# Performance work log

Measured on AMD Instinct MI355X. Metric: run time of the kernel, lower is better.

Reference implementation:

```python
import jax, jax.numpy as jnp
import numpy as np

TEMPERATURE = 0.05


def _hungarian_max(C):
    """Jonker-Volgenant shortest-augmenting-path LAP on a square numpy matrix.
    Returns col index matched to each row, maximizing total cost
    (equivalent to scipy.optimize.linear_sum_assignment(C, maximize=True))."""
    cost = -np.asarray(C, dtype=np.float64)  # minimize negated cost
    n = cost.shape[0]
    INF = np.inf
    u = np.zeros(n + 1)
    v = np.zeros(n + 1)
    p = np.zeros(n + 1, dtype=np.int64)   # p[j] = row matched to column j (1-based)
    way = np.zeros(n + 1, dtype=np.int64)
    for i in range(1, n + 1):
        p[0] = i
        j0 = 0
        minv = np.full(n + 1, INF)
        used = np.zeros(n + 1, dtype=bool)
        while True:
            used[j0] = True
            i0 = p[j0]
            delta = INF
            j1 = -1
            for j in range(1, n + 1):
                if not used[j]:
                    cur = cost[i0 - 1, j - 1] - u[i0] - v[j]
                    if cur < minv[j]:
                        minv[j] = cur
                        way[j] = j0
                    if minv[j] < delta:
                        delta = minv[j]
                        j1 = j
            for j in range(n + 1):
                if used[j]:
                    u[p[j]] += delta
                    v[j] -= delta
                else:
                    minv[j] -= delta
            j0 = j1
            if p[j0] == 0:
                break
        while j0:
            j1 = way[j0]
            p[j0] = p[j1]
            j0 = j1
    col_of_row = np.zeros(n, dtype=np.int64)
    for j in range(1, n + 1):
        col_of_row[p[j] - 1] = j - 1
    return col_of_row


def setup_inputs() -> dict:
    key = jax.random.key(0)
    k1, k2, k3 = jax.random.split(key, 3)
    B, K, D = 256, 16, 1024
    return {
        "outputs": jax.random.normal(k1, (B, K, D), dtype=jnp.float32),
        "positive_embeddings": jax.random.normal(k2, (B, K, D), dtype=jnp.float32),
        "negative_embeddings": jax.random.normal(k3, (B, K, D), dtype=jnp.float32),
    }


def reference(outputs, positive_embeddings, negative_embeddings):
    B, K, D = outputs.shape
    o = outputs.reshape(B * K, D) / TEMPERATURE          # (BK, D)
    emb = jnp.concatenate(
        [positive_embeddings.reshape(B * K, D),
         negative_embeddings.reshape(B * K, D)], axis=0)  # (2BK, D)
    sim = jnp.einsum("bd,cd->bc", o, emb)                 # (BK, 2BK)
    sim = jax.nn.log_softmax(sim, axis=1)
    # i-th KxK diagonal block: rows [K*i, K*(i+1)), cols [K*i, K*(i+1))
    idx = jnp.arange(B)
    blocks = sim.reshape(B, K, 2 * B, K)[idx, :, idx, :]  # (B, K, K)
    # Hungarian matching (detached in original -> no grad through assignment)
    blk_np = np.asarray(jax.device_get(jax.lax.stop_gradient(blocks)))
    cols = jnp.asarray(np.stack([_hungarian_max(blk_np[b]) for b in range(B)]))  # (B, K)
    matched = blocks[idx[:, None], jnp.arange(K)[None, :], cols]  # (B, K)
    # per-sample mean of -matched, then mean over batch == overall mean
    return jnp.mean(-matched)
```

## Files before the change

### kernel.cpp

```cpp
#include <hip/hip_runtime.h>
#include <hip/hip_bf16.h>
#include <math.h>

#define Ddim 1024
#define Mrows 4096
#define Ncols 8192
#define BM 128
#define BN 128
#define BK 32
#define NCS 64
#define CS 64
#define RT (Mrows / BM)
#define KITERS (Ddim / BK)
#define NSOLVE 256
#define SCALE 20.0f
#define ARR_ELEMS (Mrows * Ddim)
#define DOTS_PAD 132

typedef __bf16 bf16_t;
typedef __bf16 bf16x8 __attribute__((ext_vector_type(8)));
typedef float f32x4 __attribute__((ext_vector_type(4)));

#define LOAD16_TO_LDS(g, l)                                                  \
  __builtin_amdgcn_global_load_lds(                                          \
      (const __attribute__((address_space(1))) void*)(g),                    \
      (__attribute__((address_space(3))) void*)(l), 16, 0, 0)

__device__ __forceinline__ int rdlane_i(int v, int lane) {
  return __builtin_amdgcn_readlane(v, lane);
}
__device__ __forceinline__ float rdlane_f(float v, int lane) {
  return __int_as_float(__builtin_amdgcn_readlane(__float_as_int(v), lane));
}
__device__ __forceinline__ float rdfirst_f(float v) {
  return __int_as_float(__builtin_amdgcn_readfirstlane(__float_as_int(v)));
}

template <int N>
__device__ __forceinline__ void argmin_ror(float& cand, int& idx) {
  const float ov = __int_as_float(__builtin_amdgcn_update_dpp(
      __float_as_int(cand), __float_as_int(cand), 0x120 | N, 0xf, 0xf, false));
  const int oi = __builtin_amdgcn_update_dpp(idx, idx, 0x120 | N, 0xf, 0xf, false);
  if (ov < cand || (ov == cand && oi < idx)) { cand = ov; idx = oi; }
}

__global__ __launch_bounds__(256) void cvt_kernel(
    const float* __restrict__ o, const float* __restrict__ pos,
    const float* __restrict__ neg, bf16_t* __restrict__ ob,
    bf16_t* __restrict__ pb, bf16_t* __restrict__ nb,
    float* __restrict__ out)
{
  if (blockIdx.x == 0 && threadIdx.x == 0) out[0] = 0.f;
  const int idx = blockIdx.x * 256 + threadIdx.x;
  const int seg = idx >> 19;
  const int off = idx & ((1 << 19) - 1);
  const float* src = (seg == 0) ? o : (seg == 1) ? pos : neg;
  bf16_t* dst = (seg == 0) ? ob : (seg == 1) ? pb : nb;
  const float4 v0 = *(const float4*)(src + (size_t)off * 8);
  const float4 v1 = *(const float4*)(src + (size_t)off * 8 + 4);
  bf16x8 r = {(bf16_t)v0.x, (bf16_t)v0.y, (bf16_t)v0.z, (bf16_t)v0.w,
              (bf16_t)v1.x, (bf16_t)v1.y, (bf16_t)v1.z, (bf16_t)v1.w};
  *(bf16x8*)(dst + (size_t)off * 8) = r;
}

__global__ __launch_bounds__(256, 4) void mega_kernel(
    const bf16_t* __restrict__ ob, const bf16_t* __restrict__ pb,
    const bf16_t* __restrict__ nb, const float* __restrict__ o,
    const float* __restrict__ pos,
    float* __restrict__ pm, float* __restrict__ pl, float* __restrict__ out)
{
  __shared__ bf16_t As[2][BM * BK];
  __shared__ bf16_t Bs[2][BN * BK];
  __shared__ float Csolve[16][16];

  if (blockIdx.x < NSOLVE) {
    const int b = blockIdx.x;
    float* o_s = (float*)(&As[0][0]);
    float* p_s = (float*)(&Bs[0][0]);
    const int di = threadIdx.x >> 4;
    const int dj = threadIdx.x & 15;
    float s0 = 0.f, s1 = 0.f, s2 = 0.f, s3 = 0.f;
    for (int k0 = 0; k0 < Ddim; k0 += 128) {
      __syncthreads();
#pragma unroll
      for (int rp = 0; rp < 4; ++rp) {
        const int fid = threadIdx.x + 256 * rp;
        const int arr = fid >> 9;
        const int row = (fid >> 5) & 15;
        const int c4 = fid & 31;
        const float* src = arr ? pos : o;
        float* dst = arr ? p_s : o_s;
        const float4 v =
            *(const float4*)(src + (size_t)(b * 16 + row) * Ddim + k0 + c4 * 4);
        *(float4*)(dst + row * DOTS_PAD + c4 * 4) = v;
      }
      __syncthreads();
#pragma unroll
      for (int kk = 0; kk < 128; kk += 4) {
        const float4 a = *(const float4*)(o_s + di * DOTS_PAD + kk);
        const float4 e = *(const float4*)(p_s + dj * DOTS_PAD + kk);
        s0 = fmaf(a.x, e.x, s0); s1 = fmaf(a.y, e.y, s1);
        s2 = fmaf(a.z, e.z, s2); s3 = fmaf(a.w, e.w, s3);
      }
    }
    Csolve[di][dj] = (s0 + s1 + s2 + s3) * SCALE;
    __syncthreads();
    if (threadIdx.x >= 64) return;

    const int L = threadIdx.x;
    const float INF = 3.0e38f;
    float vj = 0.f, u_reg = 0.f;
    int pj = 0;
    float minv = INF;
    int wayj = 0;
    bool usedj = false, on_tree = false;

    for (int i = 1; i <= 16; ++i) {
      minv = INF; wayj = 0; usedj = false; on_tree = false;
      int j0 = 0;
      while (true) {
        usedj = usedj || (L + 1 == j0);
        const int i0 = (j0 == 0) ? i : rdlane_i(pj, j0 - 1);
        on_tree = on_tree || (L + 1 == i0);
        const float ui0 = rdlane_f(u_reg, i0 - 1);
        if (!usedj) {
          const float cur = -Csolve[i0 - 1][L & 15] - ui0 - vj;
          if (cur < minv) { minv = cur; wayj = j0; }
        }
        float cand = (L < 16 && !usedj) ? minv : INF;
        int idx = L;
        argmin_ror<8>(cand, idx);
        argmin_ror<4>(cand, idx);
        argmin_ror<2>(cand, idx);
        argmin_ror<1>(cand, idx);
        const float delta = rdfirst_f(cand);
        const int j1 = __builtin_amdgcn_readfirstlane(idx) + 1;
        if (usedj) vj -= delta; else minv -= delta;
        if (on_tree) u_reg += delta;
        j0 = j1;
        if (rdlane_i(pj, j0 - 1) == 0) break;
      }
      while (j0 != 0) {
        const int j1a = rdlane_i(wayj, j0 - 1);
        const int pjn = (j1a == 0) ? i : rdlane_i(pj, (j1a > 0) ? j1a - 1 : 0);
        if (L == j0 - 1) pj = pjn;
        j0 = j1a;
      }
    }

    float loss = (L < 16) ? -Csolve[pj - 1][L] : 0.f;
#pragma unroll
    for (int off = 8; off > 0; off >>= 1) loss += __shfl_down(loss, off, 64);
    if (L == 0) atomicAdd(out, loss * (1.0f / 4096.0f));
    return;
  }

  const int bid = blockIdx.x - NSOLVE;
  const int rt = bid >> 6;
  const int cs = bid & 63;
  const int row0 = rt * BM;
  const bf16_t* Eb = (cs < 32) ? (pb + (size_t)cs * BN * Ddim)
                               : (nb + (size_t)(cs - 32) * BN * Ddim);

  const int t = threadIdx.x;
  const int wave = t >> 6;
  const int lane = t & 63;
  const int quad = lane >> 4;
  const int l16 = lane & 15;
  const int koff = ((quad ^ ((l16 >> 1) & 3)) << 3);
  const int lr4 = lane >> 2;
  const int cstg = lane & 3;

  f32x4 acc[2][8];
#pragma unroll
  for (int a = 0; a < 2; ++a)
#pragma unroll
    for (int b2 = 0; b2 < 8; ++b2) acc[a][b2] = (f32x4){0.f, 0.f, 0.f, 0.f};

#pragma unroll
  for (int cl = 0; cl < 2; ++cl) {
    const int r = wave * 32 + cl * 16 + lr4;
    const int gc = cstg ^ ((r >> 1) & 3);
    LOAD16_TO_LDS(ob + (size_t)(row0 + r) * Ddim + gc * 8,
                  &As[0][(wave * 32 + cl * 16) * BK]);
    LOAD16_TO_LDS(Eb + (size_t)r * Ddim + gc * 8,
                  &Bs[0][(wave * 32 + cl * 16) * BK]);
  }

  int p = 0;
  for (int kc = 0; kc < KITERS; ++kc) {
    __syncthreads();
    if (kc + 1 < KITERS) {
      const int k0 = (kc + 1) * BK;
#pragma unroll
      for (int cl = 0; cl < 2; ++cl) {
        const int r = wave * 32 + cl * 16 + lr4;
        const int gc = cstg ^ ((r >> 1) & 3);
        LOAD16_TO_LDS(ob + (size_t)(row0 + r) * Ddim + k0 + gc * 8,
                      &As[p ^ 1][(wave * 32 + cl * 16) * BK]);
        LOAD16_TO_LDS(Eb + (size_t)r * Ddim + k0 + gc * 8,
                      &Bs[p ^ 1][(wave * 32 + cl * 16) * BK]);
      }
    }

    const int rowA0 = wave * 32 + l16;
    const bf16x8 a0 = *(const bf16x8*)(&As[p][rowA0 * BK + koff]);
    const bf16x8 a1 = *(const bf16x8*)(&As[p][(rowA0 + 16) * BK + koff]);
#pragma unroll
    for (int fn = 0; fn < 8; ++fn) {
      const bf16x8 bf = *(const bf16x8*)(&Bs[p][(fn * 16 + l16) * BK + koff]);
      acc[0][fn] = __builtin_amdgcn_mfma_f32_16x16x32_bf16(a0, bf, acc[0][fn], 0, 0, 0);
      acc[1][fn] = __builtin_amdgcn_mfma_f32_16x16x32_bf16(a1, bf, acc[1][fn], 0, 0, 0);
    }
    p ^= 1;
  }

#pragma unroll
  for (int fm = 0; fm < 2; ++fm) {
#pragma unroll
    for (int r = 0; r < 4; ++r) {
      float s[8];
#pragma unroll
      for (int fn = 0; fn < 8; ++fn) s[fn] = acc[fm][fn][r] * SCALE;
      float m = s[0];
#pragma unroll
      for (int fn = 1; fn < 8; ++fn) m = fmaxf(m, s[fn]);
#pragma unroll
      for (int off = 1; off <= 8; off <<= 1)
        m = fmaxf(m, __shfl_xor(m, off, 64));
      float l = 0.f;
#pragma unroll
      for (int fn = 0; fn < 8; ++fn) l += __expf(s[fn] - m);
#pragma unroll
      for (int off = 1; off <= 8; off <<= 1)
        l += __shfl_xor(l, off, 64);
      if (l16 == 0) {
        const int rg = row0 + wave * 32 + fm * 16 + quad * 4 + r;
        pm[(size_t)rg * CS + cs] = m;
        pl[(size_t)rg * CS + cs] = l;
      }
    }
  }
}

__global__ __launch_bounds__(256) void lse_sum_kernel(
    const float* __restrict__ pm, const float* __restrict__ pl,
    float* __restrict__ out)
{
  const int row = blockIdx.x * 4 + (threadIdx.x >> 6);
  const int lane = threadIdx.x & 63;
  const size_t base = (size_t)row * CS + lane;
  float m = pm[base];
  float l = pl[base];
#pragma unroll
  for (int off = 32; off > 0; off >>= 1) {
    const float m2 = __shfl_xor(m, off, 64);
    const float l2 = __shfl_xor(l, off, 64);
    const float M = fmaxf(m, m2);
    l = l * __expf(m - M) + l2 * __expf(m2 - M);
    m = M;
  }
  const float v = m + logf(l);
  __shared__ float wsum[4];
  if (lane == 0) wsum[threadIdx.x >> 6] = v;
  __syncthreads();
  if (threadIdx.x == 0)
    atomicAdd(out, (wsum[0] + wsum[1] + wsum[2] + wsum[3]) * (1.0f / 4096.0f));
}

extern "C" void kernel_launch(void* const* d_in, const int* in_sizes, int n_in,
                              void* d_out, int out_size, void* d_ws, size_t ws_size,
                              hipStream_t stream) {
  const float* o   = (const float*)d_in[0];
  const float* pos = (const float*)d_in[1];
  const float* neg = (const float*)d_in[2];
  float* out = (float*)d_out;

  float* ws = (float*)d_ws;
  float* pm = ws;
  float* pl = pm + (size_t)4096 * CS;
  bf16_t* ob = (bf16_t*)(pl + (size_t)4096 * CS);
  bf16_t* pb = ob + (size_t)ARR_ELEMS;
  bf16_t* nb = pb + (size_t)ARR_ELEMS;

  cvt_kernel<<<3 * ARR_ELEMS / 8 / 256, 256, 0, stream>>>(o, pos, neg, ob, pb, nb, out);
  mega_kernel<<<NSOLVE + RT * NCS, 256, 0, stream>>>(ob, pb, nb, o, pos, pm, pl, out);
  lse_sum_kernel<<<4096 / 4, 256, 0, stream>>>(pm, pl, out);
}
```

Baseline: 198.6 us.

## Use 2x2 wave tiling in GEMM tile for better LDS fragment reuse

Reorganizes the four waves of the 128x128 GEMM block from 4x1 (each wave 32 rows by 128 cols) into a 2x2 grid (each wave 64x64). Per K-step each wave now loads 8 LDS fragments instead of 10 to feed 16 MFMAs, cutting LDS read traffic. Because each wave now covers only half the columns, partial softmax max/sum are written per wave-column, doubling the partial buffer to 128 entries per row, and the LSE reduction kernel merges two entries per lane first.

After: 201.0 us. About the same (+1.2%).

```diff
diff --git a/kernel.cpp b/kernel.cpp
--- a/kernel.cpp
+++ b/kernel.cpp
@@ -9,7 +9,7 @@
 #define BN 128
 #define BK 32
 #define NCS 64
-#define CS 64
+#define CS2 128
 #define RT (Mrows / BM)
 #define KITERS (Ddim / BK)
 #define NSOLVE 256
@@ -164,6 +164,8 @@
 
   const int t = threadIdx.x;
   const int wave = t >> 6;
+  const int wr = wave >> 1;
+  const int wc = wave & 1;
   const int lane = t & 63;
   const int quad = lane >> 4;
   const int l16 = lane & 15;
@@ -171,11 +173,11 @@
   const int lr4 = lane >> 2;
   const int cstg = lane & 3;
 
-  f32x4 acc[2][8];
-#pragma unroll
-  for (int a = 0; a < 2; ++a)
-#pragma unroll
-    for (int b2 = 0; b2 < 8; ++b2) acc[a][b2] = (f32x4){0.f, 0.f, 0.f, 0.f};
+  f32x4 acc[4][4];
+#pragma unroll
+  for (int a = 0; a < 4; ++a)
+#pragma unroll
+    for (int b2 = 0; b2 < 4; ++b2) acc[a][b2] = (f32x4){0.f, 0.f, 0.f, 0.f};
 
 #pragma unroll
   for (int cl = 0; cl < 2; ++cl) {
@@ -203,41 +205,42 @@
       }
     }
 
-    const int rowA0 = wave * 32 + l16;
-    const bf16x8 a0 = *(const bf16x8*)(&As[p][rowA0 * BK + koff]);
-    const bf16x8 a1 = *(const bf16x8*)(&As[p][(rowA0 + 16) * BK + koff]);
-#pragma unroll
-    for (int fn = 0; fn < 8; ++fn) {
-      const bf16x8 bf = *(const bf16x8*)(&Bs[p][(fn * 16 + l16) * BK + koff]);
-      acc[0][fn] = __builtin_amdgcn_mfma_f32_16x16x32_bf16(a0, bf, acc[0][fn], 0, 0, 0);
-      acc[1][fn] = __builtin_amdgcn_mfma_f32_16x16x32_bf16(a1, bf, acc[1][fn], 0, 0, 0);
-    }
+    bf16x8 af[4], bg[4];
+#pragma unroll
+    for (int f = 0; f < 4; ++f) {
+      af[f] = *(const bf16x8*)(&As[p][(wr * 64 + f * 16 + l16) * BK + koff]);
+      bg[f] = *(const bf16x8*)(&Bs[p][(wc * 64 + f * 16 + l16) * BK + koff]);
+    }
+#pragma unroll
+    for (int fm = 0; fm < 4; ++fm)
+#pragma unroll
+      for (int fn = 0; fn < 4; ++fn)
+        acc[fm][fn] = __builtin_amdgcn_mfma_f32_16x16x32_bf16(
+            af[fm], bg[fn], acc[fm][fn], 0, 0, 0);
     p ^= 1;
   }
 
 #pragma unroll
-  for (int fm = 0; fm < 2; ++fm) {
+  for (int fm = 0; fm < 4; ++fm) {
 #pragma unroll
     for (int r = 0; r < 4; ++r) {
-      float s[8];
-#pragma unroll
-      for (int fn = 0; fn < 8; ++fn) s[fn] = acc[fm][fn][r] * SCALE;
-      float m = s[0];
-#pragma unroll
-      for (int fn = 1; fn < 8; ++fn) m = fmaxf(m, s[fn]);
+      float s[4];
+#pragma unroll
+      for (int fn = 0; fn < 4; ++fn) s[fn] = acc[fm][fn][r] * SCALE;
+      float m = fmaxf(fmaxf(s[0], s[1]), fmaxf(s[2], s[3]));
 #pragma unroll
       for (int off = 1; off <= 8; off <<= 1)
         m = fmaxf(m, __shfl_xor(m, off, 64));
       float l = 0.f;
 #pragma unroll
-      for (int fn = 0; fn < 8; ++fn) l += __expf(s[fn] - m);
+      for (int fn = 0; fn < 4; ++fn) l += __expf(s[fn] - m);
 #pragma unroll
       for (int off = 1; off <= 8; off <<= 1)
         l += __shfl_xor(l, off, 64);
       if (l16 == 0) {
-        const int rg = row0 + wave * 32 + fm * 16 + quad * 4 + r;
-        pm[(size_t)rg * CS + cs] = m;
-        pl[(size_t)rg * CS + cs] = l;
+        const int rg = row0 + wr * 64 + fm * 16 + quad * 4 + r;
+        pm[(size_t)rg * CS2 + cs * 2 + wc] = m;
+        pl[(size_t)rg * CS2 + cs * 2 + wc] = l;
       }
     }
   }
@@ -249,9 +252,16 @@
 {
   const int row = blockIdx.x * 4 + (threadIdx.x >> 6);
   const int lane = threadIdx.x & 63;
-  const size_t base = (size_t)row * CS + lane;
+  const size_t base = (size_t)row * CS2 + lane;
   float m = pm[base];
   float l = pl[base];
+  {
+    const float m2 = pm[base + 64];
+    const float l2 = pl[base + 64];
+    const float M = fmaxf(m, m2);
+    l = l * __expf(m - M) + l2 * __expf(m2 - M);
+    m = M;
+  }
 #pragma unroll
   for (int off = 32; off > 0; off >>= 1) {
     const float m2 = __shfl_xor(m, off, 64);
@@ -278,8 +288,8 @@
 
   float* ws = (float*)d_ws;
   float* pm = ws;
-  float* pl = pm + (size_t)4096 * CS;
-  bf16_t* ob = (bf16_t*)(pl + (size_t)4096 * CS);
+  float* pl = pm + (size_t)4096 * CS2;
+  bf16_t* ob = (bf16_t*)(pl + (size_t)4096 * CS2);
   bf16_t* pb = ob + (size_t)ARR_ELEMS;
   bf16_t* nb = pb + (size_t)ARR_ELEMS;
 
```

## Fuse fp32-to-bf16 conversion into GEMM tile loads, drop separate convert kernel

Applied to the files above, without the earlier changes.

Removes the standalone conversion kernel that rewrote all three fp32 inputs as bf16 copies. The GEMM now loads fp32 tiles into registers, converts them to bf16 and stores them into LDS, prefetching two stages ahead in registers. The async global-to-LDS loads are replaced by this register path, and the output is zeroed with a memset. In exchange each tile load moves twice the bytes from global/L2, and register pressure rises in a kernel launched with occupancy bound 4.

Result: slower. 203.9 us (+2.7%).

```diff
diff --git a/kernel.cpp b/kernel.cpp
--- a/kernel.cpp
+++ b/kernel.cpp
@@ -14,17 +14,11 @@
 #define KITERS (Ddim / BK)
 #define NSOLVE 256
 #define SCALE 20.0f
-#define ARR_ELEMS (Mrows * Ddim)
 #define DOTS_PAD 132
 
 typedef __bf16 bf16_t;
 typedef __bf16 bf16x8 __attribute__((ext_vector_type(8)));
 typedef float f32x4 __attribute__((ext_vector_type(4)));
-
-#define LOAD16_TO_LDS(g, l)                                                  \
-  __builtin_amdgcn_global_load_lds(                                          \
-      (const __attribute__((address_space(1))) void*)(g),                    \
-      (__attribute__((address_space(3))) void*)(l), 16, 0, 0)
 
 __device__ __forceinline__ int rdlane_i(int v, int lane) {
   return __builtin_amdgcn_readlane(v, lane);
@@ -44,29 +38,9 @@
   if (ov < cand || (ov == cand && oi < idx)) { cand = ov; idx = oi; }
 }
 
-__global__ __launch_bounds__(256) void cvt_kernel(
+__global__ __launch_bounds__(256, 4) void mega_kernel(
     const float* __restrict__ o, const float* __restrict__ pos,
-    const float* __restrict__ neg, bf16_t* __restrict__ ob,
-    bf16_t* __restrict__ pb, bf16_t* __restrict__ nb,
-    float* __restrict__ out)
-{
-  if (blockIdx.x == 0 && threadIdx.x == 0) out[0] = 0.f;
-  const int idx = blockIdx.x * 256 + threadIdx.x;
-  const int seg = idx >> 19;
-  const int off = idx & ((1 << 19) - 1);
-  const float* src = (seg == 0) ? o : (seg == 1) ? pos : neg;
-  bf16_t* dst = (seg == 0) ? ob : (seg == 1) ? pb : nb;
-  const float4 v0 = *(const float4*)(src + (size_t)off * 8);
-  const float4 v1 = *(const float4*)(src + (size_t)off * 8 + 4);
-  bf16x8 r = {(bf16_t)v0.x, (bf16_t)v0.y, (bf16_t)v0.z, (bf16_t)v0.w,
-              (bf16_t)v1.x, (bf16_t)v1.y, (bf16_t)v1.z, (bf16_t)v1.w};
-  *(bf16x8*)(dst + (size_t)off * 8) = r;
-}
-
-__global__ __launch_bounds__(256, 4) void mega_kernel(
-    const bf16_t* __restrict__ ob, const bf16_t* __restrict__ pb,
-    const bf16_t* __restrict__ nb, const float* __restrict__ o,
-    const float* __restrict__ pos,
+    const float* __restrict__ neg,
     float* __restrict__ pm, float* __restrict__ pl, float* __restrict__ out)
 {
   __shared__ bf16_t As[2][BM * BK];
@@ -159,8 +133,8 @@
   const int rt = bid >> 6;
   const int cs = bid & 63;
   const int row0 = rt * BM;
-  const bf16_t* Eb = (cs < 32) ? (pb + (size_t)cs * BN * Ddim)
-                               : (nb + (size_t)(cs - 32) * BN * Ddim);
+  const float* Eb = (cs < 32) ? (pos + (size_t)cs * BN * Ddim)
+                              : (neg + (size_t)(cs - 32) * BN * Ddim);
 
   const int t = threadIdx.x;
   const int wave = t >> 6;
@@ -177,31 +151,50 @@
 #pragma unroll
     for (int b2 = 0; b2 < 8; ++b2) acc[a][b2] = (f32x4){0.f, 0.f, 0.f, 0.f};
 
-#pragma unroll
-  for (int cl = 0; cl < 2; ++cl) {
-    const int r = wave * 32 + cl * 16 + lr4;
-    const int gc = cstg ^ ((r >> 1) & 3);
-    LOAD16_TO_LDS(ob + (size_t)(row0 + r) * Ddim + gc * 8,
-                  &As[0][(wave * 32 + cl * 16) * BK]);
-    LOAD16_TO_LDS(Eb + (size_t)r * Ddim + gc * 8,
-                  &Bs[0][(wave * 32 + cl * 16) * BK]);
-  }
+  float4 ra[2][2], rb[2][2];
+
+#define STAGE_LOAD(k0)                                                       \
+  {                                                                          \
+    _Pragma("unroll")                                                        \
+    for (int cl = 0; cl < 2; ++cl) {                                         \
+      const int r = wave * 32 + cl * 16 + lr4;                               \
+      const int gc = cstg ^ ((r >> 1) & 3);                                  \
+      const float* pa = o + (size_t)(row0 + r) * Ddim + (k0) + gc * 8;       \
+      const float* pe = Eb + (size_t)r * Ddim + (k0) + gc * 8;               \
+      ra[cl][0] = *(const float4*)(pa);                                      \
+      ra[cl][1] = *(const float4*)(pa + 4);                                  \
+      rb[cl][0] = *(const float4*)(pe);                                      \
+      rb[cl][1] = *(const float4*)(pe + 4);                                  \
+    }                                                                        \
+  }
+
+#define STAGE_WRITE(pp)                                                      \
+  {                                                                          \
+    _Pragma("unroll")                                                        \
+    for (int cl = 0; cl < 2; ++cl) {                                         \
+      const int r = wave * 32 + cl * 16 + lr4;                               \
+      const bf16x8 va = {(bf16_t)ra[cl][0].x, (bf16_t)ra[cl][0].y,           \
+                         (bf16_t)ra[cl][0].z, (bf16_t)ra[cl][0].w,           \
+                         (bf16_t)ra[cl][1].x, (bf16_t)ra[cl][1].y,           \
+                         (bf16_t)ra[cl][1].z, (bf16_t)ra[cl][1].w};          \
+      const bf16x8 vb = {(bf16_t)rb[cl][0].x, (bf16_t)rb[cl][0].y,           \
+                         (bf16_t)rb[cl][0].z, (bf16_t)rb[cl][0].w,           \
+                         (bf16_t)rb[cl][1].x, (bf16_t)rb[cl][1].y,           \
+                         (bf16_t)rb[cl][1].z, (bf16_t)rb[cl][1].w};          \
+      *(bf16x8*)(&As[pp][r * BK + cstg * 8]) = va;                           \
+      *(bf16x8*)(&Bs[pp][r * BK + cstg * 8]) = vb;                           \
+    }                                                                        \
+  }
+
+  STAGE_LOAD(0);
+  STAGE_WRITE(0);
+  STAGE_LOAD(BK);
+  __syncthreads();
 
   int p = 0;
   for (int kc = 0; kc < KITERS; ++kc) {
-    __syncthreads();
-    if (kc + 1 < KITERS) {
-      const int k0 = (kc + 1) * BK;
-#pragma unroll
-      for (int cl = 0; cl < 2; ++cl) {
-        const int r = wave * 32 + cl * 16 + lr4;
-        const int gc = cstg ^ ((r >> 1) & 3);
-        LOAD16_TO_LDS(ob + (size_t)(row0 + r) * Ddim + k0 + gc * 8,
-                      &As[p ^ 1][(wave * 32 + cl * 16) * BK]);
-        LOAD16_TO_LDS(Eb + (size_t)r * Ddim + k0 + gc * 8,
-                      &Bs[p ^ 1][(wave * 32 + cl * 16) * BK]);
-      }
-    }
+    if (kc + 1 < KITERS) STAGE_WRITE(p ^ 1);
+    if (kc + 2 < KITERS) STAGE_LOAD((kc + 2) * BK);
 
     const int rowA0 = wave * 32 + l16;
     const bf16x8 a0 = *(const bf16x8*)(&As[p][rowA0 * BK + koff]);
@@ -212,6 +205,7 @@
       acc[0][fn] = __builtin_amdgcn_mfma_f32_16x16x32_bf16(a0, bf, acc[0][fn], 0, 0, 0);
       acc[1][fn] = __builtin_amdgcn_mfma_f32_16x16x32_bf16(a1, bf, acc[1][fn], 0, 0, 0);
     }
+    if (kc + 1 < KITERS) __syncthreads();
     p ^= 1;
   }
 
@@ -241,6 +235,8 @@
       }
     }
   }
+#undef STAGE_LOAD
+#undef STAGE_WRITE
 }
 
 __global__ __launch_bounds__(256) void lse_sum_kernel(
@@ -279,11 +275,8 @@
   float* ws = (float*)d_ws;
   float* pm = ws;
   float* pl = pm + (size_t)4096 * CS;
-  bf16_t* ob = (bf16_t*)(pl + (size_t)4096 * CS);
-  bf16_t* pb = ob + (size_t)ARR_ELEMS;
-  bf16_t* nb = pb + (size_t)ARR_ELEMS;
-
-  cvt_kernel<<<3 * ARR_ELEMS / 8 / 256, 256, 0, stream>>>(o, pos, neg, ob, pb, nb, out);
-  mega_kernel<<<NSOLVE + RT * NCS, 256, 0, stream>>>(ob, pb, nb, o, pos, pm, pl, out);
+
+  hipMemsetAsync(out, 0, sizeof(float), stream);
+  mega_kernel<<<NSOLVE + RT * NCS, 256, 0, stream>>>(o, pos, neg, pm, pl, out);
   lse_sum_kernel<<<4096 / 4, 256, 0, stream>>>(pm, pl, out);
 }
```
